# Kernel optimization log

Hardware: AMD Instinct MI355X
Metric: run time of the kernel (lower is better)

Reference implementation:

```python
import jax, jax.numpy as jnp
import numpy as np

HEADS = 9
MODEL_DIM = 256
LN_EPS = 1e-5


def _relative_features(h, w):
    # grid[i, j] = (i, j); rel[i, j, k, l] = (k - i, l - j)
    r = jnp.arange(h if h >= w else w)
    gi, gj = jnp.meshgrid(jnp.arange(h), jnp.arange(w), indexing='ij')
    grid = jnp.stack([gi, gj], axis=-1).astype(jnp.float32)          # (h, w, 2)
    rel = grid[None, None, :, :, :] - grid[:, :, None, None, :]       # (h, w, h, w, 2)
    cross = (rel[..., 0] * rel[..., 1])[..., None]
    return jnp.concatenate([rel, rel ** 2, cross], axis=-1)           # (h, w, h, w, 5)


def _layer_norm(x, gamma, beta):
    mu = jnp.mean(x, axis=-1, keepdims=True)
    var = jnp.var(x, axis=-1, keepdims=True)
    return (x - mu) * jax.lax.rsqrt(var + LN_EPS) * gamma + beta


def setup_inputs() -> dict:
    key = jax.random.key(0)
    ks = jax.random.split(key, 6)
    bs, h, w = 16, 32, 32
    hidden_state = jax.random.normal(ks[0], (bs, h, w, MODEL_DIM), dtype=jnp.float32)
    attention_centers = 2.0 * jax.random.normal(ks[1], (HEADS, 2), dtype=jnp.float32)
    attention_spreads = jnp.eye(2, dtype=jnp.float32)[None] + 0.01 * jax.random.normal(
        ks[2], (HEADS, 2, 2), dtype=jnp.float32)
    # torch Linear(in=heads*model_dim, out=model_dim): weight (out, in)
    fan_in = HEADS * MODEL_DIM
    bound = 1.0 / np.sqrt(fan_in)
    value_w = jax.random.uniform(ks[3], (MODEL_DIM, fan_in), jnp.float32, -bound, bound)
    value_b = jax.random.uniform(ks[4], (MODEL_DIM,), jnp.float32, -bound, bound)
    ln_gamma = jnp.ones((MODEL_DIM,), jnp.float32)
    ln_beta = jnp.zeros((MODEL_DIM,), jnp.float32)
    return {
        'hidden_state': hidden_state,
        'attention_centers': attention_centers,
        'attention_spreads': attention_spreads,
        'value_w': value_w,
        'value_b': value_b,
        'ln_gamma': ln_gamma,
        'ln_beta': ln_beta,
    }


def reference(hidden_state, attention_centers, attention_spreads, value_w, value_b,
              ln_gamma, ln_beta):
    bs, h, w, d = hidden_state.shape
    # pre_norm=True: normalize first, residual uses normalized hidden (as in source)
    x = _layer_norm(hidden_state, ln_gamma, ln_beta)

    # per-head quadratic target vector u (faithful to source, incl. the (c + mu_2) term)
    inv_cov = jnp.einsum('hij,hkj->hik', attention_spreads, attention_spreads)
    a, b, c = inv_cov[:, 0, 0], inv_cov[:, 0, 1], inv_cov[:, 1, 1]
    mu1, mu2 = attention_centers[:, 0], attention_centers[:, 1]
    u = -0.5 * jnp.stack(
        [-2 * (a * mu1 + b * mu2), -2 * (c + mu2 + b * mu1), a, c, 2 * b], axis=-1)  # (H, 5)

    R = _relative_features(h, w)                                      # (h, w, h, w, 5)
    scores = jnp.einsum('ijkld,hd->ijhkl', R, u)                      # (h, w, H, h, w)
    probs = jax.nn.softmax(scores.reshape(h, w, HEADS, h * w), axis=-1)
    probs = probs.reshape(h, w, HEADS, h, w)
    # dropout prob = 0 (eval mode)

    context = jnp.einsum('ijhkl,bkld->bijhd', probs, x)               # (bs, h, w, H, d)
    context = context.reshape(bs, h, w, HEADS * d)
    output = context @ value_w.T + value_b
    output = output + x
    return output, probs
```

## Files before the change

kernel.cpp:

```cpp
#include <hip/hip_runtime.h>
#include <hip/hip_bf16.h>
#include <stdint.h>

typedef __bf16 bf16;
typedef __bf16 bf16x4 __attribute__((ext_vector_type(4)));
typedef __bf16 bf16x8 __attribute__((ext_vector_type(8)));
typedef float  f32x4  __attribute__((ext_vector_type(4)));

#define GLDS16(g, l) __builtin_amdgcn_global_load_lds(                      \
    (const __attribute__((address_space(1))) void*)(g),                     \
    (__attribute__((address_space(3))) void*)(l), 16, 0, 0)

#define BARX() do { __builtin_amdgcn_s_barrier();                            \
                    __builtin_amdgcn_sched_barrier(0); } while (0)
#define VMW(n) do { asm volatile("s_waitcnt vmcnt(" #n ")" ::: "memory");    \
                    __builtin_amdgcn_sched_barrier(0); } while (0)

#define TRUNC_S 18.0f

__global__ __launch_bounds__(256) void k_ln(const float* __restrict__ hs,
                                            const float* __restrict__ gamma,
                                            const float* __restrict__ beta,
                                            bf16* __restrict__ xb) {
  int wid = threadIdx.x >> 6, lane = threadIdx.x & 63;
  size_t row = (size_t)blockIdx.x * 4 + wid;
  const float4* p = (const float4*)(hs + row * 256);
  float4 v = p[lane];
  float s  = v.x + v.y + v.z + v.w;
  float s2 = v.x*v.x + v.y*v.y + v.z*v.z + v.w*v.w;
#pragma unroll
  for (int o = 32; o; o >>= 1) { s += __shfl_xor(s, o); s2 += __shfl_xor(s2, o); }
  float mu  = s * (1.0f/256.0f);
  float var = s2 * (1.0f/256.0f) - mu*mu;
  float rs  = rsqrtf(var + 1e-5f);
  float4 g = ((const float4*)gamma)[lane];
  float4 b = ((const float4*)beta)[lane];
  bf16x4 o4;
  o4[0] = (bf16)((v.x - mu) * rs * g.x + b.x);
  o4[1] = (bf16)((v.y - mu) * rs * g.y + b.y);
  o4[2] = (bf16)((v.z - mu) * rs * g.z + b.z);
  o4[3] = (bf16)((v.w - mu) * rs * g.w + b.w);
  *(bf16x4*)(xb + row * 256 + lane * 4) = o4;
}

__global__ __launch_bounds__(256) void k_xt(const bf16* __restrict__ xb,
                                            bf16* __restrict__ xt) {
  __shared__ bf16 tile[64][65];
  int kl0 = blockIdx.x * 64, d0 = blockIdx.y * 64, b = blockIdx.z;
  int t = threadIdx.x;
  int r = t >> 2, c0 = (t & 3) * 16;
  const bf16* src = xb + ((size_t)(b * 1024 + kl0 + r)) * 256 + d0 + c0;
  bf16x8 v0 = *(const bf16x8*)src;
  bf16x8 v1 = *(const bf16x8*)(src + 8);
#pragma unroll
  for (int i = 0; i < 8; i++) { tile[r][c0 + i] = v0[i]; tile[r][c0 + 8 + i] = v1[i]; }
  __syncthreads();
  int dr = t >> 2, k0 = (t & 3) * 16;
  bf16x8 w0, w1;
#pragma unroll
  for (int i = 0; i < 8; i++) { w0[i] = tile[k0 + i][dr]; w1[i] = tile[k0 + 8 + i][dr]; }
  bf16* dst = xt + ((size_t)(b * 256 + d0 + dr)) * 1024 + kl0 + k0;
  *(bf16x8*)dst = w0;
  *(bf16x8*)(dst + 8) = w1;
}

__global__ __launch_bounds__(256) void k_vwb(const float* __restrict__ vw,
                                             bf16* __restrict__ vwb,
                                             const float* __restrict__ centers,
                                             const float* __restrict__ spreads,
                                             int* __restrict__ sorted) {
  __shared__ int nt[72];
  int t = threadIdx.x;
  if (blockIdx.x == 288) {
    if (t < 72) {
      int h = t >> 3, mb = t & 7;
      float S00 = spreads[h*4+0], S01 = spreads[h*4+1];
      float S10 = spreads[h*4+2], S11 = spreads[h*4+3];
      float a_ = S00*S00 + S01*S01;
      float b_ = S00*S10 + S01*S11;
      float c_ = S10*S10 + S11*S11;
      float mu1 = centers[h*2+0], mu2 = centers[h*2+1];
      float det = fmaxf(a_*c_ - b_*b_, 1e-6f);
      float A_ = a_*mu1 + b_*mu2;
      float B_ = c_ + mu2 + b_*mu1;
      float ustar = (c_*A_ - b_*B_) / det;
      float lam = fmaxf(a_ - b_*b_/c_, 1e-3f);
      float M_ = __fsqrt_rn(TRUNC_S / lam) + 1.5f;
      float lo_f = (float)(mb*4) + ustar, hi_f = lo_f + 3.0f;
      int k_lo = (int)floorf(fminf(lo_f, 31.0f) - M_);
      int k_hi = (int)ceilf(fmaxf(hi_f, 0.0f) + M_) + 1;
      if (k_lo < 0) k_lo = 0;
      if (k_hi > 32) k_hi = 32;
      if (k_hi <= k_lo) { k_lo = 0; k_hi = 32; }
      nt[t] = k_hi - k_lo;
    }
    __syncthreads();
    if (t < 72) {
      int my = nt[t], r = 0;
#pragma unroll 1
      for (int j = 0; j < 72; j++) {
        int v = nt[j];
        if (v > my || (v == my && j < t)) r++;
      }
      sorted[r] = t;
    }
    return;
  }
  int i = (blockIdx.x * 256 + t) * 8;
  float4 q0 = *(const float4*)(vw + i);
  float4 q1 = *(const float4*)(vw + i + 4);
  bf16x8 o;
  o[0]=(bf16)q0.x; o[1]=(bf16)q0.y; o[2]=(bf16)q0.z; o[3]=(bf16)q0.w;
  o[4]=(bf16)q1.x; o[5]=(bf16)q1.y; o[6]=(bf16)q1.z; o[7]=(bf16)q1.w;
  *(bf16x8*)(vwb + i) = o;
}

__global__ __launch_bounds__(256) void k_probs(const float* __restrict__ centers,
                                               const float* __restrict__ spreads,
                                               float* __restrict__ pf,
                                               bf16* __restrict__ pb2) {
  int bid = blockIdx.x;
  int h  = bid % 9;
  int ij = bid / 9;
  int i = ij >> 5, j = ij & 31;
  float S00 = spreads[h*4+0], S01 = spreads[h*4+1];
  float S10 = spreads[h*4+2], S11 = spreads[h*4+3];
  float a  = S00*S00 + S01*S01;
  float bq = S00*S10 + S01*S11;
  float c  = S10*S10 + S11*S11;
  float mu1 = centers[h*2+0], mu2 = centers[h*2+1];
  float u0 = a*mu1 + bq*mu2;
  float u1 = c + mu2 + bq*mu1;
  float u2 = -0.5f*a, u3 = -0.5f*c, u4 = -bq;
  int t = threadIdx.x;
  float sc[4]; float mx = -1e30f;
#pragma unroll
  for (int s = 0; s < 4; s++) {
    int kl = t*4 + s;
    float d0 = (float)((kl >> 5) - i);
    float d1 = (float)((kl & 31) - j);
    float v = d0*(u0 + u2*d0) + d1*(u1 + u3*d1) + u4*d0*d1;
    sc[s] = v; mx = fmaxf(mx, v);
  }
  __shared__ float red[8];
#pragma unroll
  for (int o = 32; o; o >>= 1) mx = fmaxf(mx, __shfl_xor(mx, o));
  int lane = t & 63, wid = t >> 6;
  if (lane == 0) red[wid] = mx;
  __syncthreads();
  mx = fmaxf(fmaxf(red[0], red[1]), fmaxf(red[2], red[3]));
  float sum = 0.f;
#pragma unroll
  for (int s = 0; s < 4; s++) { sc[s] = __expf(sc[s] - mx); sum += sc[s]; }
#pragma unroll
  for (int o = 32; o; o >>= 1) sum += __shfl_xor(sum, o);
  if (lane == 0) red[4 + wid] = sum;
  __syncthreads();
  sum = red[4] + red[5] + red[6] + red[7];
  float inv = 1.0f / sum;
  float4 o;
  o.x = sc[0]*inv; o.y = sc[1]*inv; o.z = sc[2]*inv; o.w = sc[3]*inv;
  *(float4*)(pf + (size_t)bid*1024 + t*4) = o;
  bf16x4 ob;
  ob[0] = (bf16)o.x; ob[1] = (bf16)o.y; ob[2] = (bf16)o.z; ob[3] = (bf16)o.w;
  *(bf16x4*)(pb2 + ((size_t)(h*32 + (t >> 3))*1024 + ij)*32 + (t & 7)*4) = ob;
}

__device__ __forceinline__ bf16x8 frag_ld(const bf16* base, int row, int g) {
  return *(const bf16x8*)(base + row*32 + ((g ^ ((row >> 1) & 3)) << 3));
}

__global__ __launch_bounds__(256, 2) void k_ctx(const bf16* __restrict__ pb2,
                                                const bf16* __restrict__ xt,
                                                const float* __restrict__ centers,
                                                const float* __restrict__ spreads,
                                                const int* __restrict__ sorted,
                                                bf16* __restrict__ ctx,
                                                int b0, int nbt) {
  __shared__ bf16 Bs[3*8192];
  int r_  = blockIdx.x / nbt;
  int nb  = blockIdx.x % nbt;
  int cls = sorted[r_];
  int h   = cls >> 3;
  int mb  = cls & 7;
  int ij0 = mb * 128;
  int nrow0 = (b0 + nb) * 256;

  int t = threadIdx.x, lane = t & 63, w = t >> 6;
  int wr = w >> 1, wc = w & 1;
  int g = lane >> 4, rl = lane & 15;

  float S00 = spreads[h*4+0], S01 = spreads[h*4+1];
  float S10 = spreads[h*4+2], S11 = spreads[h*4+3];
  float a_ = S00*S00 + S01*S01;
  float b_ = S00*S10 + S01*S11;
  float c_ = S10*S10 + S11*S11;
  float mu1 = centers[h*2+0], mu2 = centers[h*2+1];
  float det = fmaxf(a_*c_ - b_*b_, 1e-6f);
  float A_ = a_*mu1 + b_*mu2;
  float B_ = c_ + mu2 + b_*mu1;
  float ustar = (c_*A_ - b_*B_) / det;
  float lam = fmaxf(a_ - b_*b_/c_, 1e-3f);
  float M_ = __fsqrt_rn(TRUNC_S / lam) + 1.5f;
  float lo_f = (float)(mb*4) + ustar, hi_f = lo_f + 3.0f;
  int k_lo = (int)floorf(fminf(lo_f, 31.0f) - M_);
  int k_hi = (int)ceilf(fmaxf(hi_f, 0.0f) + M_) + 1;
  if (k_lo < 0) k_lo = 0;
  if (k_hi > 32) k_hi = 32;
  if (k_hi <= k_lo) { k_lo = 0; k_hi = 32; }
  const int NT = k_hi - k_lo;

  f32x4 acc[4][8];
#pragma unroll
  for (int x_ = 0; x_ < 4; x_++)
#pragma unroll
    for (int y_ = 0; y_ < 8; y_++) acc[x_][y_] = (f32x4){0.f,0.f,0.f,0.f};

  int arow = t >> 2;
  int acs  = (t & 3) ^ ((t >> 3) & 3);
  const bf16* b1 = xt + (size_t)(nrow0 + arow) * 1024 + k_lo*32 + acs * 8;
  const bf16* aP = pb2 + ((size_t)(h*32 + k_lo)*1024 + ij0 + wr*64 + rl)*32 + g*8;

#define STG(sb, kt) do {                                                    \
    _Pragma("unroll")                                                       \
    for (int q = 0; q < 4; q++)                                             \
      GLDS16(b1 + (size_t)q*64*1024 + (kt)*32,                              \
             ((char*)Bs) + (sb)*16384 + q*4096 + t*16);                     \
  } while (0)

#define LOADA(AF, kt) do {                                                  \
    const bf16* a_p = aP + (size_t)(kt)*32768;                              \
    _Pragma("unroll")                                                       \
    for (int fr = 0; fr < 4; fr++)                                          \
      AF[fr] = *(const bf16x8*)(a_p + fr*512);                              \
  } while (0)

#define MFM(AF, BF) do {                                                    \
    _Pragma("unroll")                                                       \
    for (int fr = 0; fr < 4; fr++)                                          \
      _Pragma("unroll")                                                     \
      for (int fn = 0; fn < 8; fn++)                                        \
        acc[fr][fn] = __builtin_amdgcn_mfma_f32_16x16x32_bf16(              \
            AF[fr], BF[fn], acc[fr][fn], 0, 0, 0);                          \
  } while (0)

  bf16x8 afA[4], afB[4];
  STG(0, 0);
  if (NT > 1) STG(1, 1);
  __builtin_amdgcn_sched_barrier(0);
  LOADA(afA, 0);
  if (NT > 1) VMW(8); else VMW(4);
  BARX();

  int cur = 0, kt = 0;
  while (true) {
    {
      bf16x8 bf_[8];
#pragma unroll
      for (int fn = 0; fn < 8; fn++) bf_[fn] = frag_ld(Bs + cur*8192, wc*128 + fn*16 + rl, g);
      int sb = cur + 2; if (sb >= 3) sb -= 3;
      if (kt + 2 < NT) STG(sb, kt + 2);
      __builtin_amdgcn_sched_barrier(0);
      if (kt + 1 < NT) LOADA(afB, kt + 1);
      MFM(afA, bf_);
      if (kt + 1 >= NT) break;
      if (kt + 2 < NT) VMW(8); else VMW(4);
      BARX();
      cur = cur + 1; if (cur >= 3) cur = 0;
      kt++;
    }
    {
      bf16x8 bf_[8];
#pragma unroll
      for (int fn = 0; fn < 8; fn++) bf_[fn] = frag_ld(Bs + cur*8192, wc*128 + fn*16 + rl, g);
      int sb = cur + 2; if (sb >= 3) sb -= 3;
      if (kt + 2 < NT) STG(sb, kt + 2);
      __builtin_amdgcn_sched_barrier(0);
      if (kt + 1 < NT) LOADA(afA, kt + 1);
      MFM(afB, bf_);
      if (kt + 1 >= NT) break;
      if (kt + 2 < NT) VMW(8); else VMW(4);
      BARX();
      cur = cur + 1; if (cur >= 3) cur = 0;
      kt++;
    }
  }
#undef STG
#undef LOADA
#undef MFM

#pragma unroll
  for (int fr = 0; fr < 4; fr++) {
    int row = ij0 + wr*64 + fr*16 + g*4;
#pragma unroll
    for (int fn = 0; fn < 8; fn++) {
      int d = wc*128 + fn*16 + rl;
      size_t base = ((size_t)nb*1024 + row) * 2304 + h*256 + d;
      f32x4 a4 = acc[fr][fn];
#pragma unroll
      for (int r = 0; r < 4; r++)
        ctx[base + (size_t)r*2304] = (bf16)a4[r];
    }
  }
}

__global__ __launch_bounds__(512, 1) void k_out(const bf16* __restrict__ ctx,
                                                const bf16* __restrict__ vwb,
                                                const bf16* __restrict__ xb,
                                                const float* __restrict__ vbias,
                                                float* __restrict__ out, int b0) {
  __shared__ bf16 lds[3 * 20480];
  int t = threadIdx.x, lane = t & 63, w = t >> 6;
  int wr = w >> 2, wc = w & 3;
  int g = lane >> 4, rl = lane & 15;
  int r0 = blockIdx.x * 64;
  char* ldsb = (char*)lds;

  f32x4 acc[2][4];
#pragma unroll
  for (int x_ = 0; x_ < 2; x_++)
#pragma unroll
    for (int y_ = 0; y_ < 4; y_++) acc[x_][y_] = (f32x4){0.f,0.f,0.f,0.f};

  int rr  = t >> 3;
  int csw = (t & 7) ^ (rr & 7);
  const bf16* aS = ctx + (size_t)(r0 + rr) * 2304 + csw * 8;
  const bf16* bS = vwb + (size_t)rr * 2304 + csw * 8;

#define STGO(sb, kt) do {                                                     \
    GLDS16(aS + (kt)*64, ldsb + (sb)*40960 + t*16);                           \
    _Pragma("unroll")                                                         \
    for (int q = 0; q < 4; q++)                                               \
      GLDS16(bS + (size_t)q*64*2304 + (kt)*64,                                \
             ldsb + (sb)*40960 + 8192 + q*8192 + t*16);                       \
  } while (0)

  STGO(0, 0); STGO(1, 1);
  VMW(5);
  BARX();

  int cur = 0;
  for (int kt = 0; kt < 36; ++kt) {
    int sb = cur + 2; if (sb >= 3) sb -= 3;
    const char* ab = ldsb + cur*40960;
    const char* bb = ab + 8192;
    bf16x8 af0[2], af1[2], bf0[4], bf1[4];
#pragma unroll
    for (int fr = 0; fr < 2; fr++) {
      int row_ = wr*32 + fr*16 + rl;
      af0[fr] = *(const bf16x8*)(ab + row_*128 + (((g  ) ^ (row_&7)) << 4));
      af1[fr] = *(const bf16x8*)(ab + row_*128 + (((g+4) ^ (row_&7)) << 4));
    }
#pragma unroll
    for (int fn = 0; fn < 4; fn++) {
      int row_ = wc*64 + fn*16 + rl;
      bf0[fn] = *(const bf16x8*)(bb + row_*128 + (((g  ) ^ (row_&7)) << 4));
      bf1[fn] = *(const bf16x8*)(bb + row_*128 + (((g+4) ^ (row_&7)) << 4));
    }
    if (kt + 2 < 36) STGO(sb, kt + 2);
    BARX();
    __builtin_amdgcn_s_setprio(1);
#pragma unroll
    for (int fr = 0; fr < 2; fr++)
#pragma unroll
      for (int fn = 0; fn < 4; fn++) {
        acc[fr][fn] = __builtin_amdgcn_mfma_f32_16x16x32_bf16(af0[fr], bf0[fn], acc[fr][fn], 0, 0, 0);
        acc[fr][fn] = __builtin_amdgcn_mfma_f32_16x16x32_bf16(af1[fr], bf1[fn], acc[fr][fn], 0, 0, 0);
      }
    __builtin_amdgcn_s_setprio(0);
    if (kt + 2 < 36)      VMW(5);
    else if (kt + 1 < 36) VMW(0);
    BARX();
    cur = cur + 1; if (cur >= 3) cur = 0;
  }
#undef STGO

#pragma unroll
  for (int fr = 0; fr < 2; fr++) {
    int rowl = r0 + wr*32 + fr*16 + g*4;
    size_t rowg = (size_t)b0*1024 + rowl;
#pragma unroll
    for (int fn = 0; fn < 4; fn++) {
      int m = wc*64 + fn*16 + rl;
      float bv = vbias[m];
      size_t base = rowg*256 + m;
#pragma unroll
      for (int r = 0; r < 4; r++)
        out[base + (size_t)r*256] = acc[fr][fn][r] + bv + (float)xb[base + (size_t)r*256];
    }
  }
}

extern "C" void kernel_launch(void* const* d_in, const int* in_sizes, int n_in,
                              void* d_out, int out_size, void* d_ws, size_t ws_size,
                              hipStream_t stream) {
  const float* hs      = (const float*)d_in[0];
  const float* centers = (const float*)d_in[1];
  const float* spreads = (const float*)d_in[2];
  const float* vw      = (const float*)d_in[3];
  const float* vb      = (const float*)d_in[4];
  const float* gamma   = (const float*)d_in[5];
  const float* beta    = (const float*)d_in[6];
  float* out     = (float*)d_out;
  float* probs_f = out + 4194304;

  char* ws = (char*)d_ws;
  bf16* xb  = (bf16*)ws;
  bf16* pb2 = (bf16*)(ws + 8388608);
  bf16* xt  = (bf16*)(ws + 27262976);
  bf16* vwb = (bf16*)(ws + 35651584);
  bf16* ctx = (bf16*)(ws + 36831232);

  int CB = 16;
  while (CB > 1 && 36831232ull + (size_t)CB * 4718592ull + 512ull > ws_size) CB >>= 1;
  int* sortedp = (int*)(ws + 36831232 + (size_t)CB * 4718592ull);

  k_ln<<<4096, 256, 0, stream>>>(hs, gamma, beta, xb);
  k_xt<<<dim3(16, 4, 16), 256, 0, stream>>>(xb, xt);
  k_probs<<<9216, 256, 0, stream>>>(centers, spreads, probs_f, pb2);
  k_vwb<<<289, 256, 0, stream>>>(vw, vwb, centers, spreads, sortedp);
  for (int b0 = 0; b0 < 16; b0 += CB) {
    int c = (16 - b0) < CB ? (16 - b0) : CB;
    k_ctx<<<dim3(72 * c), 256, 0, stream>>>(pb2, xt, centers, spreads, sortedp, ctx, b0, c);
    k_out<<<dim3(c*16), 512, 0, stream>>>(ctx, vwb, xb, vb, out, b0);
  }
}
```

Before: 109.3 us.

## Fuse LayerNorm with transpose and tighten softmax truncation threshold

Merges the LayerNorm kernel and the separate bf16 transpose kernel into one kernel that normalizes 32 rows per block, writes the row-major result, and transposes via shared memory into the d-major buffer. This drops one launch and one re-read of the normalized activations from global memory. It also lowers the probability truncation threshold TRUNC_S from 18 to 14, which likely shrinks the key region the context kernel visits but risks dropping more small softmax mass.

```diff
diff --git a/kernel.cpp b/kernel.cpp
--- a/kernel.cpp
+++ b/kernel.cpp
@@ -16,52 +16,48 @@
 #define VMW(n) do { asm volatile("s_waitcnt vmcnt(" #n ")" ::: "memory");    \
                     __builtin_amdgcn_sched_barrier(0); } while (0)
 
-#define TRUNC_S 18.0f
-
-__global__ __launch_bounds__(256) void k_ln(const float* __restrict__ hs,
-                                            const float* __restrict__ gamma,
-                                            const float* __restrict__ beta,
-                                            bf16* __restrict__ xb) {
-  int wid = threadIdx.x >> 6, lane = threadIdx.x & 63;
-  size_t row = (size_t)blockIdx.x * 4 + wid;
-  const float4* p = (const float4*)(hs + row * 256);
-  float4 v = p[lane];
-  float s  = v.x + v.y + v.z + v.w;
-  float s2 = v.x*v.x + v.y*v.y + v.z*v.z + v.w*v.w;
-#pragma unroll
-  for (int o = 32; o; o >>= 1) { s += __shfl_xor(s, o); s2 += __shfl_xor(s2, o); }
-  float mu  = s * (1.0f/256.0f);
-  float var = s2 * (1.0f/256.0f) - mu*mu;
-  float rs  = rsqrtf(var + 1e-5f);
-  float4 g = ((const float4*)gamma)[lane];
-  float4 b = ((const float4*)beta)[lane];
-  bf16x4 o4;
-  o4[0] = (bf16)((v.x - mu) * rs * g.x + b.x);
-  o4[1] = (bf16)((v.y - mu) * rs * g.y + b.y);
-  o4[2] = (bf16)((v.z - mu) * rs * g.z + b.z);
-  o4[3] = (bf16)((v.w - mu) * rs * g.w + b.w);
-  *(bf16x4*)(xb + row * 256 + lane * 4) = o4;
-}
-
-__global__ __launch_bounds__(256) void k_xt(const bf16* __restrict__ xb,
-                                            bf16* __restrict__ xt) {
-  __shared__ bf16 tile[64][65];
-  int kl0 = blockIdx.x * 64, d0 = blockIdx.y * 64, b = blockIdx.z;
-  int t = threadIdx.x;
-  int r = t >> 2, c0 = (t & 3) * 16;
-  const bf16* src = xb + ((size_t)(b * 1024 + kl0 + r)) * 256 + d0 + c0;
-  bf16x8 v0 = *(const bf16x8*)src;
-  bf16x8 v1 = *(const bf16x8*)(src + 8);
-#pragma unroll
-  for (int i = 0; i < 8; i++) { tile[r][c0 + i] = v0[i]; tile[r][c0 + 8 + i] = v1[i]; }
+#define TRUNC_S 14.0f
+
+__global__ __launch_bounds__(256) void k_lnt(const float* __restrict__ hs,
+                                             const float* __restrict__ gamma,
+                                             const float* __restrict__ beta,
+                                             bf16* __restrict__ xb,
+                                             bf16* __restrict__ xt) {
+  __shared__ bf16 tile[4][32][66];
+  int kl0 = blockIdx.x * 32, b = blockIdx.y;
+  int t = threadIdx.x, lane = t & 63, w = t >> 6;
+  float4 g  = ((const float4*)gamma)[lane];
+  float4 be = ((const float4*)beta)[lane];
+  int sq = lane >> 4, col = (lane & 15) * 4;
+#pragma unroll
+  for (int i = 0; i < 8; i++) {
+    int r = w * 8 + i;
+    size_t row = (size_t)b * 1024 + kl0 + r;
+    float4 v = ((const float4*)(hs + row * 256))[lane];
+    float s  = v.x + v.y + v.z + v.w;
+    float s2 = v.x*v.x + v.y*v.y + v.z*v.z + v.w*v.w;
+#pragma unroll
+    for (int o = 32; o; o >>= 1) { s += __shfl_xor(s, o); s2 += __shfl_xor(s2, o); }
+    float mu = s * (1.0f/256.0f);
+    float var = s2 * (1.0f/256.0f) - mu*mu;
+    float rs = rsqrtf(var + 1e-5f);
+    bf16x4 o4;
+    o4[0] = (bf16)((v.x - mu) * rs * g.x + be.x);
+    o4[1] = (bf16)((v.y - mu) * rs * g.y + be.y);
+    o4[2] = (bf16)((v.z - mu) * rs * g.z + be.z);
+    o4[3] = (bf16)((v.w - mu) * rs * g.w + be.w);
+    *(bf16x4*)(xb + row * 256 + lane * 4) = o4;
+    *(bf16x4*)(&tile[sq][r][col]) = o4;
+  }
   __syncthreads();
-  int dr = t >> 2, k0 = (t & 3) * 16;
-  bf16x8 w0, w1;
-#pragma unroll
-  for (int i = 0; i < 8; i++) { w0[i] = tile[k0 + i][dr]; w1[i] = tile[k0 + 8 + i][dr]; }
-  bf16* dst = xt + ((size_t)(b * 256 + d0 + dr)) * 1024 + kl0 + k0;
-  *(bf16x8*)dst = w0;
-  *(bf16x8*)(dst + 8) = w1;
+  int dr = t >> 2, k0 = (t & 3) * 8;
+#pragma unroll
+  for (int q = 0; q < 4; q++) {
+    bf16x8 w0;
+#pragma unroll
+    for (int i = 0; i < 8; i++) w0[i] = tile[q][k0 + i][dr];
+    *(bf16x8*)(xt + ((size_t)(b * 256 + q * 64 + dr)) * 1024 + kl0 + k0) = w0;
+  }
 }
 
 __global__ __launch_bounds__(256) void k_vwb(const float* __restrict__ vw,
@@ -415,8 +411,7 @@
   while (CB > 1 && 36831232ull + (size_t)CB * 4718592ull + 512ull > ws_size) CB >>= 1;
   int* sortedp = (int*)(ws + 36831232 + (size_t)CB * 4718592ull);
 
-  k_ln<<<4096, 256, 0, stream>>>(hs, gamma, beta, xb);
-  k_xt<<<dim3(16, 4, 16), 256, 0, stream>>>(xb, xt);
+  k_lnt<<<dim3(32, 16), 256, 0, stream>>>(hs, gamma, beta, xb, xt);
   k_probs<<<9216, 256, 0, stream>>>(centers, spreads, probs_f, pb2);
   k_vwb<<<289, 256, 0, stream>>>(vw, vwb, centers, spreads, sortedp);
   for (int b0 = 0; b0 < 16; b0 += CB) {
```

After: 103.3 us. -5.5%, faster.
